# Optimization experiments

Measured on AMD Instinct MI355X. Metric: run time of the kernel, lower is better.

Reference implementation:

```python
import jax, jax.numpy as jnp
import numpy as np

B, S, D, N = 8, 2048, 1024, 1024
RMIN, RMAX = 0.9, 0.999
MAX_PHASE = 6.2831853
EPS = 1e-5


def _ln(v):
    # LayerNorm without affine params (elementwise_affine=False)
    mu = jnp.mean(v, axis=-1, keepdims=True)
    var = jnp.var(v, axis=-1, keepdims=True)
    return (v - mu) * jax.lax.rsqrt(var + EPS)


def setup_inputs() -> dict:
    key = jax.random.key(0)
    ks = jax.random.split(key, 12)
    x = jax.random.normal(ks[0], (B, S, D), dtype=jnp.float32)
    hidden_re = jnp.zeros((B, N), dtype=jnp.float32)
    hidden_im = jnp.zeros((B, N), dtype=jnp.float32)
    # LRU ring initialization (Orvieto et al. 2023)
    u1 = jax.random.uniform(ks[1], (N,), dtype=jnp.float32)
    u2 = jax.random.uniform(ks[2], (N,), dtype=jnp.float32)
    nu_log = jnp.log(-0.5 * jnp.log(u1 * (RMAX**2 - RMIN**2) + RMIN**2))
    theta_log = jnp.log(MAX_PHASE * u2)
    B_re = jax.random.normal(ks[3], (N, D), dtype=jnp.float32) / np.sqrt(2 * D)
    B_im = jax.random.normal(ks[4], (N, D), dtype=jnp.float32) / np.sqrt(2 * D)
    C_re = jax.random.normal(ks[5], (N, N), dtype=jnp.float32) / np.sqrt(N)
    C_im = jax.random.normal(ks[6], (N, N), dtype=jnp.float32) / np.sqrt(N)
    D_skip = jax.random.normal(ks[7], (N, D), dtype=jnp.float32) / np.sqrt(D)
    W_gate = jax.random.normal(ks[8], (N, D), dtype=jnp.float32) / np.sqrt(D)  # gating_proj
    W_con = jax.random.normal(ks[9], (D, N), dtype=jnp.float32) / np.sqrt(N)   # contract
    return {"x": x, "hidden_re": hidden_re, "hidden_im": hidden_im,
            "nu_log": nu_log, "theta_log": theta_log,
            "B_re": B_re, "B_im": B_im, "C_re": C_re, "C_im": C_im,
            "D_skip": D_skip, "W_gate": W_gate, "W_con": W_con}


def reference(x, hidden_re, hidden_im, nu_log, theta_log,
              B_re, B_im, C_re, C_im, D_skip, W_gate, W_con):
    residual = x
    # diagonal complex transition lambda and input normalizer gamma
    mag = jnp.exp(-jnp.exp(nu_log))                 # |lambda|, [N]
    phase = jnp.exp(theta_log)
    lam_re = mag * jnp.cos(phase)
    lam_im = mag * jnp.sin(phase)
    gamma = jnp.sqrt(1.0 - mag * mag)               # sqrt(1-|lambda|^2)
    # input projection (complex), pre-scaled by gamma: [B,S,N]
    u_re = jnp.einsum("bsd,nd->bsn", x, B_re) * gamma
    u_im = jnp.einsum("bsd,nd->bsn", x, B_im) * gamma
    # sequential linear recurrence h_t = lambda * h_{t-1} + u_t (complex)
    def step(h, u):
        h_re, h_im = h
        ur, ui = u
        nr = lam_re * h_re - lam_im * h_im + ur
        ni = lam_re * h_im + lam_im * h_re + ui
        return (nr, ni), (nr, ni)
    (hf_re, hf_im), (hs_re, hs_im) = jax.lax.scan(
        step, (hidden_re, hidden_im),
        (jnp.swapaxes(u_re, 0, 1), jnp.swapaxes(u_im, 0, 1)))  # time-major [S,B,N]
    hs_re = jnp.swapaxes(hs_re, 0, 1)  # [B,S,N]
    hs_im = jnp.swapaxes(hs_im, 0, 1)
    # y = Re(C h) + D x
    y = (jnp.einsum("bsn,mn->bsm", hs_re, C_re)
         - jnp.einsum("bsn,mn->bsm", hs_im, C_im)
         + jnp.einsum("bsd,md->bsm", x, D_skip))
    # gated norm / MLP fusion
    y = _ln(y)                                              # rnn_post_norm
    gate = jax.nn.gelu(_ln(jnp.einsum("bsd,nd->bsn", residual, W_gate)), approximate=False)
    y = y * gate
    y = jax.nn.gelu(_ln(y), approximate=False)              # contract_norm + activation
    out = jnp.einsum("bsn,dn->bsd", y, W_con)               # contract
    return (out, hf_re, hf_im)
```

## Files before the change

kernel.cpp:

```cpp
#include <hip/hip_runtime.h>
#include <math.h>

#define Bsz 8
#define Ssz 2048
#define Dsz 1024
#define Nsz 1024
#define CHUNKS 64
#define CLEN 32
#define Msz (Bsz * Ssz)

typedef unsigned short u16;
typedef __attribute__((ext_vector_type(8))) short short8;
typedef __attribute__((ext_vector_type(4))) float floatx4;

__device__ __forceinline__ float b2f(u16 u) {
    unsigned v = ((unsigned)u) << 16; float f; __builtin_memcpy(&f, &v, 4); return f;
}
__device__ __forceinline__ u16 f2b(float f) {
    unsigned u; __builtin_memcpy(&u, &f, 4);
    unsigned r = u + 0x7fffu + ((u >> 16) & 1u);
    return (u16)(r >> 16);
}

struct CvtJobs {
    const float* src[8];
    u16* dst[8];
    int n4[8];
    float scale[8];
    int blk_start[9];
};

__global__ __launch_bounds__(256)
void cvt_multi(CvtJobs J) {
    int b = blockIdx.x;
    int j = 0;
    #pragma unroll
    for (int t = 0; t < 7; ++t) if (b >= J.blk_start[t + 1]) j = t + 1;
    int i = (b - J.blk_start[j]) * 256 + threadIdx.x;
    if (i < J.n4[j]) {
        float4 v = ((const float4*)J.src[j])[i];
        float s = J.scale[j];
        ushort4 o;
        o.x = f2b(v.x * s); o.y = f2b(v.y * s);
        o.z = f2b(v.z * s); o.w = f2b(v.w * s);
        ((ushort4*)J.dst[j])[i] = o;
    }
}

__global__ void lam_setup(const float* __restrict__ nu_log, const float* __restrict__ theta_log,
                          float* lam_re, float* lam_im, float* gam,
                          float* lamL_re, float* lamL_im) {
    int n = blockIdx.x * 256 + threadIdx.x;
    if (n >= Nsz) return;
    float mag = expf(-expf(nu_log[n]));
    float ph  = expf(theta_log[n]);
    float lr = mag * cosf(ph), li = mag * sinf(ph);
    lam_re[n] = lr; lam_im[n] = li;
    gam[n] = sqrtf(fmaxf(1.0f - mag * mag, 0.0f));
    float ar = lr, ai = li;
    #pragma unroll
    for (int i = 0; i < 5; ++i) { float nr = ar*ar - ai*ai; float ni = 2.0f*ar*ai; ar = nr; ai = ni; }
    lamL_re[n] = ar; lamL_im[n] = ai;
}

#define BM 128
#define BN 128
#define BK 64

struct GemmJob {
    const u16* A0; const u16* W0;
    const u16* A1; const u16* W1;
    const u16* A2; const u16* W2;
    int P;
    float* outF;
    u16*   outB;
    const float* colscale;
};
struct GemmBatch { GemmJob j[3]; };

__global__ __launch_bounds__(256, 2)
void gemm_bt(GemmBatch batch, int M, int N, int K) {
    const GemmJob job = batch.j[blockIdx.z];
    __shared__ u16 As[BM * BK];
    __shared__ u16 Ws[BN * BK];
    const int tid  = threadIdx.x;
    const int wave = tid >> 6, lane = tid & 63;
    const int bm = blockIdx.x, bn = blockIdx.y;
    const int wm = (wave >> 1) * 64, wn = (wave & 1) * 64;

    floatx4 acc[4][4];
    #pragma unroll
    for (int i = 0; i < 4; ++i)
        #pragma unroll
        for (int j = 0; j < 4; ++j) acc[i][j] = (floatx4){0.f, 0.f, 0.f, 0.f};

    const u16* Aps[3] = { job.A0, job.A1, job.A2 };
    const u16* Wps[3] = { job.W0, job.W1, job.W2 };

    const int srow8 = lane >> 3;
    const int scol  = ((lane & 7) ^ srow8) * 8;
    const int frow = lane & 15;
    const int fq   = lane >> 4;
    const int fsw  = frow & 7;

    for (int p = 0; p < job.P; ++p) {
        const u16* A = Aps[p];
        const u16* W = Wps[p];
        const u16* gAb = A + (size_t)(bm * BM + srow8) * K + scol;
        const u16* gWb = W + (size_t)(bn * BN + srow8) * K + scol;
        for (int kk = 0; kk < K; kk += BK) {
            __syncthreads();
            #pragma unroll
            for (int jj = 0; jj < 4; ++jj) {
                const int row0 = wave * 32 + jj * 8;
                const u16* gA = gAb + (size_t)row0 * K + kk;
                const u16* gW = gWb + (size_t)row0 * K + kk;
                u16* lA = As + row0 * BK;
                u16* lW = Ws + row0 * BK;
                __builtin_amdgcn_global_load_lds((const __attribute__((address_space(1))) void*)gA,
                                                 (__attribute__((address_space(3))) void*)lA, 16, 0, 0);
                __builtin_amdgcn_global_load_lds((const __attribute__((address_space(1))) void*)gW,
                                                 (__attribute__((address_space(3))) void*)lW, 16, 0, 0);
            }
            __syncthreads();
            #pragma unroll
            for (int h = 0; h < 2; ++h) {
                const int ca = ((h << 2) | fq) ^ fsw;
                short8 af[4], wf[4];
                #pragma unroll
                for (int i = 0; i < 4; ++i)
                    af[i] = *(const short8*)(As + (wm + i * 16 + frow) * BK + ca * 8);
                #pragma unroll
                for (int i = 0; i < 4; ++i)
                    wf[i] = *(const short8*)(Ws + (wn + i * 16 + frow) * BK + ca * 8);
                #pragma unroll
                for (int mi = 0; mi < 4; ++mi)
                    #pragma unroll
                    for (int ni = 0; ni < 4; ++ni)
                        acc[mi][ni] = __builtin_amdgcn_mfma_f32_16x16x32_bf16(af[mi], wf[ni], acc[mi][ni], 0, 0, 0);
            }
        }
    }

    const int rgrp = lane >> 4;
    const int ccol = lane & 15;
    #pragma unroll
    for (int mi = 0; mi < 4; ++mi) {
        #pragma unroll
        for (int r = 0; r < 4; ++r) {
            int row = bm * BM + wm + mi * 16 + rgrp * 4 + r;
            #pragma unroll
            for (int ni = 0; ni < 4; ++ni) {
                int col = bn * BN + wn + ni * 16 + ccol;
                float v = acc[mi][ni][r];
                if (job.colscale) v *= job.colscale[col];
                size_t idx = (size_t)row * N + col;
                if (job.outF) job.outF[idx] = v;
                else          job.outB[idx] = f2b(v);
            }
        }
    }
}

__global__ void scan_phase1(const u16* __restrict__ u_re, const u16* __restrict__ u_im,
                            const float* __restrict__ lam_re, const float* __restrict__ lam_im,
                            float* __restrict__ carry_re, float* __restrict__ carry_im) {
    int n = blockIdx.x * 256 + threadIdx.x;
    int c = blockIdx.y, b = blockIdx.z;
    float lr = lam_re[n], li = lam_im[n];
    size_t base = ((size_t)b * Ssz + (size_t)c * CLEN) * Nsz + n;
    float hr = 0.f, hi = 0.f;
    #pragma unroll
    for (int t = 0; t < CLEN; ++t) {
        float ur = b2f(u_re[base + (size_t)t * Nsz]);
        float ui = b2f(u_im[base + (size_t)t * Nsz]);
        float nr = fmaf(lr, hr, fmaf(-li, hi, ur));
        float ni = fmaf(lr, hi, fmaf( li, hr, ui));
        hr = nr; hi = ni;
    }
    size_t ci = ((size_t)b * CHUNKS + c) * Nsz + n;
    carry_re[ci] = hr; carry_im[ci] = hi;
}

__global__ void scan_phase2(const float* __restrict__ carry_re, const float* __restrict__ carry_im,
                            const float* __restrict__ lamL_re, const float* __restrict__ lamL_im,
                            const float* __restrict__ hid_re, const float* __restrict__ hid_im,
                            float* __restrict__ entry_re, float* __restrict__ entry_im,
                            float* __restrict__ out_base) {
    int n = blockIdx.x * 256 + threadIdx.x;
    int b = blockIdx.y;
    float Lr = lamL_re[n], Li = lamL_im[n];
    float Hr = hid_re[b * Nsz + n], Hi = hid_im[b * Nsz + n];
    for (int c = 0; c < CHUNKS; ++c) {
        size_t ci = ((size_t)b * CHUNKS + c) * Nsz + n;
        entry_re[ci] = Hr; entry_im[ci] = Hi;
        float cr = carry_re[ci], cim = carry_im[ci];
        float nr = fmaf(Lr, Hr, fmaf(-Li, Hi, cr));
        float ni = fmaf(Lr, Hi, fmaf( Li, Hr, cim));
        Hr = nr; Hi = ni;
    }
    out_base[(size_t)16777216 + (size_t)b * Nsz + n] = Hr;
    out_base[(size_t)16777216 + 8192 + (size_t)b * Nsz + n] = Hi;
}

__global__ void scan_phase3(const u16* __restrict__ u_re, const u16* __restrict__ u_im,
                            const float* __restrict__ lam_re, const float* __restrict__ lam_im,
                            const float* __restrict__ entry_re, const float* __restrict__ entry_im,
                            u16* __restrict__ hs_re, u16* __restrict__ hs_im) {
    int n = blockIdx.x * 256 + threadIdx.x;
    int c = blockIdx.y, b = blockIdx.z;
    float lr = lam_re[n], li = lam_im[n];
    size_t ci = ((size_t)b * CHUNKS + c) * Nsz + n;
    float hr = entry_re[ci], hi = entry_im[ci];
    size_t base = ((size_t)b * Ssz + (size_t)c * CLEN) * Nsz + n;
    #pragma unroll
    for (int t = 0; t < CLEN; ++t) {
        float ur = b2f(u_re[base + (size_t)t * Nsz]);
        float ui = b2f(u_im[base + (size_t)t * Nsz]);
        float nr = fmaf(lr, hr, fmaf(-li, hi, ur));
        float ni = fmaf(lr, hi, fmaf( li, hr, ui));
        hr = nr; hi = ni;
        hs_re[base + (size_t)t * Nsz] = f2b(hr);
        hs_im[base + (size_t)t * Nsz] = f2b(hi);
    }
}

__device__ __forceinline__ float waveReduce(float v) {
    #pragma unroll
    for (int off = 32; off > 0; off >>= 1) v += __shfl_down(v, off, 64);
    return v;
}
__device__ __forceinline__ float gelu_exact(float x) {
    return 0.5f * x * (1.0f + erff(x * 0.70710678118654752f));
}

__global__ __launch_bounds__(256)
void fuse_ln(const u16* __restrict__ y_raw, const u16* __restrict__ gate_pre, u16* __restrict__ y3) {
    int row = blockIdx.x;
    int tid = threadIdx.x;
    int wave = tid >> 6, lane = tid & 63;
    size_t base = (size_t)row * Nsz + tid * 4;
    ushort4 yv = *(const ushort4*)(y_raw + base);
    ushort4 gv = *(const ushort4*)(gate_pre + base);
    float y[4] = { b2f(yv.x), b2f(yv.y), b2f(yv.z), b2f(yv.w) };
    float g[4] = { b2f(gv.x), b2f(gv.y), b2f(gv.z), b2f(gv.w) };

    float sy = 0.f, sy2 = 0.f, sg = 0.f, sg2 = 0.f;
    #pragma unroll
    for (int i = 0; i < 4; ++i) {
        sy += y[i]; sy2 += y[i] * y[i];
        sg += g[i]; sg2 += g[i] * g[i];
    }
    __shared__ float sh[16];
    sy = waveReduce(sy); sy2 = waveReduce(sy2);
    sg = waveReduce(sg); sg2 = waveReduce(sg2);
    if (lane == 0) { sh[wave] = sy; sh[wave + 4] = sy2; sh[wave + 8] = sg; sh[wave + 12] = sg2; }
    __syncthreads();
    sy  = sh[0] + sh[1] + sh[2] + sh[3];
    sy2 = sh[4] + sh[5] + sh[6] + sh[7];
    sg  = sh[8] + sh[9] + sh[10] + sh[11];
    sg2 = sh[12] + sh[13] + sh[14] + sh[15];
    const float inv = 1.0f / (float)Nsz;
    float muy = sy * inv, vary = sy2 * inv - muy * muy, ry = rsqrtf(vary + 1e-5f);
    float mug = sg * inv, varg = sg2 * inv - mug * mug, rg = rsqrtf(varg + 1e-5f);

    float y2[4]; float s2 = 0.f, s22 = 0.f;
    #pragma unroll
    for (int i = 0; i < 4; ++i) {
        float ly = (y[i] - muy) * ry;
        float lg = (g[i] - mug) * rg;
        float t = ly * gelu_exact(lg);
        y2[i] = t; s2 += t; s22 += t * t;
    }
    s2 = waveReduce(s2); s22 = waveReduce(s22);
    __syncthreads();
    if (lane == 0) { sh[wave] = s2; sh[wave + 4] = s22; }
    __syncthreads();
    s2  = sh[0] + sh[1] + sh[2] + sh[3];
    s22 = sh[4] + sh[5] + sh[6] + sh[7];
    float mu2 = s2 * inv, var2 = s22 * inv - mu2 * mu2, r2 = rsqrtf(var2 + 1e-5f);
    ushort4 ov;
    ov.x = f2b(gelu_exact((y2[0] - mu2) * r2));
    ov.y = f2b(gelu_exact((y2[1] - mu2) * r2));
    ov.z = f2b(gelu_exact((y2[2] - mu2) * r2));
    ov.w = f2b(gelu_exact((y2[3] - mu2) * r2));
    *(ushort4*)(y3 + base) = ov;
}

extern "C" void kernel_launch(void* const* d_in, const int* in_sizes, int n_in,
                              void* d_out, int out_size, void* d_ws, size_t ws_size,
                              hipStream_t stream) {
    const float* x         = (const float*)d_in[0];
    const float* hid_re    = (const float*)d_in[1];
    const float* hid_im    = (const float*)d_in[2];
    const float* nu_log    = (const float*)d_in[3];
    const float* theta_log = (const float*)d_in[4];
    const float* B_re      = (const float*)d_in[5];
    const float* B_im      = (const float*)d_in[6];
    const float* C_re      = (const float*)d_in[7];
    const float* C_im      = (const float*)d_in[8];
    const float* D_skip    = (const float*)d_in[9];
    const float* W_gate    = (const float*)d_in[10];
    const float* W_con     = (const float*)d_in[11];
    float* out = (float*)d_out;

    char* ws = (char*)d_ws;
    const size_t MB = 1ull << 20;
    u16* wBre  = (u16*)(ws + 0 * MB);
    u16* wBim  = (u16*)(ws + 2 * MB);
    u16* wCre  = (u16*)(ws + 4 * MB);
    u16* wCimN = (u16*)(ws + 6 * MB);
    u16* wDsk  = (u16*)(ws + 8 * MB);
    u16* wWg   = (u16*)(ws + 10 * MB);
    u16* wWc   = (u16*)(ws + 12 * MB);
    float* lam_re = (float*)(ws + 14 * MB);
    float* lam_im = lam_re + 1024;
    float* gam    = lam_re + 2048;
    float* lamLre = lam_re + 3072;
    float* lamLim = lam_re + 4096;
    u16* xb    = (u16*)(ws + 16 * MB);
    u16* u_re  = (u16*)(ws + 48 * MB);
    u16* u_im  = (u16*)(ws + 80 * MB);
    u16* gate  = (u16*)(ws + 112 * MB);
    u16* hs_re = (u16*)(ws + 144 * MB);
    u16* hs_im = (u16*)(ws + 176 * MB);
    float* carry_re = (float*)(ws + 208 * MB);
    float* carry_im = (float*)(ws + 210 * MB);
    float* entry_re = (float*)(ws + 212 * MB);
    float* entry_im = (float*)(ws + 214 * MB);
    u16* y_raw = u_re;
    u16* y3    = u_im;

    CvtJobs J = {};
    const int WQ = (Nsz * Dsz) / 4;
    const int WB = WQ / 256;
    J.src[0] = x;      J.dst[0] = xb;    J.n4[0] = (Msz * Dsz) / 4; J.scale[0] = 1.0f;
    J.src[1] = B_re;   J.dst[1] = wBre;  J.n4[1] = WQ; J.scale[1] = 1.0f;
    J.src[2] = B_im;   J.dst[2] = wBim;  J.n4[2] = WQ; J.scale[2] = 1.0f;
    J.src[3] = C_re;   J.dst[3] = wCre;  J.n4[3] = WQ; J.scale[3] = 1.0f;
    J.src[4] = C_im;   J.dst[4] = wCimN; J.n4[4] = WQ; J.scale[4] = -1.0f;
    J.src[5] = D_skip; J.dst[5] = wDsk;  J.n4[5] = WQ; J.scale[5] = 1.0f;
    J.src[6] = W_gate; J.dst[6] = wWg;   J.n4[6] = WQ; J.scale[6] = 1.0f;
    J.src[7] = W_con;  J.dst[7] = wWc;   J.n4[7] = WQ; J.scale[7] = 1.0f;
    J.blk_start[0] = 0;
    J.blk_start[1] = 16384;
    for (int t = 2; t <= 8; ++t) J.blk_start[t] = J.blk_start[t - 1] + WB;
    cvt_multi<<<J.blk_start[8], 256, 0, stream>>>(J);
    lam_setup<<<4, 256, 0, stream>>>(nu_log, theta_log, lam_re, lam_im, gam, lamLre, lamLim);

    GemmBatch b1 = {};
    b1.j[0] = { xb, wBre, nullptr, nullptr, nullptr, nullptr, 1, nullptr, u_re, gam };
    b1.j[1] = { xb, wBim, nullptr, nullptr, nullptr, nullptr, 1, nullptr, u_im, gam };
    b1.j[2] = { xb, wWg,  nullptr, nullptr, nullptr, nullptr, 1, nullptr, gate, nullptr };
    gemm_bt<<<dim3(Msz / BM, Nsz / BN, 3), 256, 0, stream>>>(b1, Msz, Nsz, Dsz);

    scan_phase1<<<dim3(Nsz / 256, CHUNKS, Bsz), 256, 0, stream>>>(u_re, u_im, lam_re, lam_im, carry_re, carry_im);
    scan_phase2<<<dim3(Nsz / 256, Bsz), 256, 0, stream>>>(carry_re, carry_im, lamLre, lamLim,
                                                          hid_re, hid_im, entry_re, entry_im, out);
    scan_phase3<<<dim3(Nsz / 256, CHUNKS, Bsz), 256, 0, stream>>>(u_re, u_im, lam_re, lam_im,
                                                                  entry_re, entry_im, hs_re, hs_im);

    GemmBatch b2 = {};
    b2.j[0] = { hs_re, wCre, hs_im, wCimN, xb, wDsk, 3, nullptr, y_raw, nullptr };
    gemm_bt<<<dim3(Msz / BM, Nsz / BN, 1), 256, 0, stream>>>(b2, Msz, Nsz, Nsz);

    fuse_ln<<<Msz, 256, 0, stream>>>(y_raw, gate, y3);

    GemmBatch b3 = {};
    b3.j[0] = { y3, wWc, nullptr, nullptr, nullptr, nullptr, 1, out, nullptr, nullptr };
    gemm_bt<<<dim3(Msz / BM, Dsz / BN, 1), 256, 0, stream>>>(b3, Msz, Dsz, Nsz);

    (void)in_sizes; (void)n_in; (void)out_size; (void)ws_size;
}
```

Measured before the change: 505.0 us.

## Double-buffer GEMM LDS tiles with BK=32 and vectorize scan kernels

```diff
diff --git a/kernel.cpp b/kernel.cpp
--- a/kernel.cpp
+++ b/kernel.cpp
@@ -8,6 +8,7 @@
 #define CHUNKS 64
 #define CLEN 32
 #define Msz (Bsz * Ssz)
+#define Ksz 1024
 
 typedef unsigned short u16;
 typedef __attribute__((ext_vector_type(8))) short short8;
@@ -65,7 +66,8 @@
 
 #define BM 128
 #define BN 128
-#define BK 64
+#define BK 32
+#define KITER 32
 
 struct GemmJob {
     const u16* A0; const u16* W0;
@@ -78,11 +80,11 @@
 };
 struct GemmBatch { GemmJob j[3]; };
 
-__global__ __launch_bounds__(256, 2)
-void gemm_bt(GemmBatch batch, int M, int N, int K) {
+__global__ __launch_bounds__(256, 3)
+void gemm_bt(GemmBatch batch) {
     const GemmJob job = batch.j[blockIdx.z];
-    __shared__ u16 As[BM * BK];
-    __shared__ u16 Ws[BN * BK];
+    __shared__ u16 As[2][BM * BK];
+    __shared__ u16 Ws[2][BN * BK];
     const int tid  = threadIdx.x;
     const int wave = tid >> 6, lane = tid & 63;
     const int bm = blockIdx.x, bn = blockIdx.y;
@@ -96,50 +98,61 @@
 
     const u16* Aps[3] = { job.A0, job.A1, job.A2 };
     const u16* Wps[3] = { job.W0, job.W1, job.W2 };
-
-    const int srow8 = lane >> 3;
-    const int scol  = ((lane & 7) ^ srow8) * 8;
+    const int TOT = job.P * KITER;
+
+    const int srow = wave * 32 + (lane >> 2);
+    const int scol = ((lane & 3) ^ ((lane >> 3) & 3)) * 8;
+    const size_t sAoff = (size_t)(bm * BM + srow) * Ksz + scol;
+    const size_t sWoff = (size_t)(bn * BN + srow) * Ksz + scol;
     const int frow = lane & 15;
-    const int fq   = lane >> 4;
-    const int fsw  = frow & 7;
-
-    for (int p = 0; p < job.P; ++p) {
-        const u16* A = Aps[p];
-        const u16* W = Wps[p];
-        const u16* gAb = A + (size_t)(bm * BM + srow8) * K + scol;
-        const u16* gWb = W + (size_t)(bn * BN + srow8) * K + scol;
-        for (int kk = 0; kk < K; kk += BK) {
-            __syncthreads();
+    const int fk   = (((lane >> 4) ^ ((frow >> 1) & 3))) * 8;
+
+    {
+        const u16* gA = Aps[0] + sAoff;
+        const u16* gW = Wps[0] + sWoff;
+        #pragma unroll
+        for (int jj = 0; jj < 2; ++jj) {
+            u16* lA = &As[0][(wave * 32 + jj * 16) * BK];
+            u16* lW = &Ws[0][(wave * 32 + jj * 16) * BK];
+            __builtin_amdgcn_global_load_lds((const __attribute__((address_space(1))) void*)(gA + (size_t)(jj * 16) * Ksz),
+                                             (__attribute__((address_space(3))) void*)lA, 16, 0, 0);
+            __builtin_amdgcn_global_load_lds((const __attribute__((address_space(1))) void*)(gW + (size_t)(jj * 16) * Ksz),
+                                             (__attribute__((address_space(3))) void*)lW, 16, 0, 0);
+        }
+    }
+
+    for (int i = 0; i < TOT; ++i) {
+        const int cur = i & 1;
+        __syncthreads();
+        if (i + 1 < TOT) {
+            const int ni = i + 1;
+            const int p = ni >> 5;
+            const int koff = (ni & 31) * BK;
+            const u16* gA = Aps[p] + sAoff + koff;
+            const u16* gW = Wps[p] + sWoff + koff;
+            const int nb = cur ^ 1;
             #pragma unroll
-            for (int jj = 0; jj < 4; ++jj) {
-                const int row0 = wave * 32 + jj * 8;
-                const u16* gA = gAb + (size_t)row0 * K + kk;
-                const u16* gW = gWb + (size_t)row0 * K + kk;
-                u16* lA = As + row0 * BK;
-                u16* lW = Ws + row0 * BK;
-                __builtin_amdgcn_global_load_lds((const __attribute__((address_space(1))) void*)gA,
+            for (int jj = 0; jj < 2; ++jj) {
+                u16* lA = &As[nb][(wave * 32 + jj * 16) * BK];
+                u16* lW = &Ws[nb][(wave * 32 + jj * 16) * BK];
+                __builtin_amdgcn_global_load_lds((const __attribute__((address_space(1))) void*)(gA + (size_t)(jj * 16) * Ksz),
                                                  (__attribute__((address_space(3))) void*)lA, 16, 0, 0);
-                __builtin_amdgcn_global_load_lds((const __attribute__((address_space(1))) void*)gW,
+                __builtin_amdgcn_global_load_lds((const __attribute__((address_space(1))) void*)(gW + (size_t)(jj * 16) * Ksz),
                                                  (__attribute__((address_space(3))) void*)lW, 16, 0, 0);
             }
-            __syncthreads();
+        }
+        short8 af[4], wf[4];
+        #pragma unroll
+        for (int t = 0; t < 4; ++t)
+            af[t] = *(const short8*)(&As[cur][(wm + t * 16 + frow) * BK + fk]);
+        #pragma unroll
+        for (int t = 0; t < 4; ++t)
+            wf[t] = *(const short8*)(&Ws[cur][(wn + t * 16 + frow) * BK + fk]);
+        #pragma unroll
+        for (int mi = 0; mi < 4; ++mi)
             #pragma unroll
-            for (int h = 0; h < 2; ++h) {
-                const int ca = ((h << 2) | fq) ^ fsw;
-                short8 af[4], wf[4];
-                #pragma unroll
-                for (int i = 0; i < 4; ++i)
-                    af[i] = *(const short8*)(As + (wm + i * 16 + frow) * BK + ca * 8);
-                #pragma unroll
-                for (int i = 0; i < 4; ++i)
-                    wf[i] = *(const short8*)(Ws + (wn + i * 16 + frow) * BK + ca * 8);
-                #pragma unroll
-                for (int mi = 0; mi < 4; ++mi)
-                    #pragma unroll
-                    for (int ni = 0; ni < 4; ++ni)
-                        acc[mi][ni] = __builtin_amdgcn_mfma_f32_16x16x32_bf16(af[mi], wf[ni], acc[mi][ni], 0, 0, 0);
-            }
-        }
+            for (int ni2 = 0; ni2 < 4; ++ni2)
+                acc[mi][ni2] = __builtin_amdgcn_mfma_f32_16x16x32_bf16(af[mi], wf[ni2], acc[mi][ni2], 0, 0, 0);
     }
 
     const int rgrp = lane >> 4;
@@ -154,7 +167,7 @@
                 int col = bn * BN + wn + ni * 16 + ccol;
                 float v = acc[mi][ni][r];
                 if (job.colscale) v *= job.colscale[col];
-                size_t idx = (size_t)row * N + col;
+                size_t idx = (size_t)row * Nsz + col;
                 if (job.outF) job.outF[idx] = v;
                 else          job.outB[idx] = f2b(v);
             }
@@ -165,21 +178,29 @@
 __global__ void scan_phase1(const u16* __restrict__ u_re, const u16* __restrict__ u_im,
                             const float* __restrict__ lam_re, const float* __restrict__ lam_im,
                             float* __restrict__ carry_re, float* __restrict__ carry_im) {
-    int n = blockIdx.x * 256 + threadIdx.x;
-    int c = blockIdx.y, b = blockIdx.z;
-    float lr = lam_re[n], li = lam_im[n];
+    int n = threadIdx.x * 4;
+    int c = blockIdx.x, b = blockIdx.y;
+    float4 lr = *(const float4*)(lam_re + n);
+    float4 li = *(const float4*)(lam_im + n);
     size_t base = ((size_t)b * Ssz + (size_t)c * CLEN) * Nsz + n;
-    float hr = 0.f, hi = 0.f;
+    float hr[4] = {0.f, 0.f, 0.f, 0.f}, hi[4] = {0.f, 0.f, 0.f, 0.f};
+    const float* lrp = (const float*)&lr; const float* lip = (const float*)&li;
     #pragma unroll
     for (int t = 0; t < CLEN; ++t) {
-        float ur = b2f(u_re[base + (size_t)t * Nsz]);
-        float ui = b2f(u_im[base + (size_t)t * Nsz]);
-        float nr = fmaf(lr, hr, fmaf(-li, hi, ur));
-        float ni = fmaf(lr, hi, fmaf( li, hr, ui));
-        hr = nr; hi = ni;
+        ushort4 urv = *(const ushort4*)(u_re + base + (size_t)t * Nsz);
+        ushort4 uiv = *(const ushort4*)(u_im + base + (size_t)t * Nsz);
+        float ur[4] = { b2f(urv.x), b2f(urv.y), b2f(urv.z), b2f(urv.w) };
+        float ui[4] = { b2f(uiv.x), b2f(uiv.y), b2f(uiv.z), b2f(uiv.w) };
+        #pragma unroll
+        for (int q = 0; q < 4; ++q) {
+            float nr = fmaf(lrp[q], hr[q], fmaf(-lip[q], hi[q], ur[q]));
+            float ni = fmaf(lrp[q], hi[q], fmaf( lip[q], hr[q], ui[q]));
+            hr[q] = nr; hi[q] = ni;
+        }
     }
     size_t ci = ((size_t)b * CHUNKS + c) * Nsz + n;
-    carry_re[ci] = hr; carry_im[ci] = hi;
+    *(float4*)(carry_re + ci) = (float4){hr[0], hr[1], hr[2], hr[3]};
+    *(float4*)(carry_im + ci) = (float4){hi[0], hi[1], hi[2], hi[3]};
 }
 
 __global__ void scan_phase2(const float* __restrict__ carry_re, const float* __restrict__ carry_im,
@@ -207,21 +228,33 @@
                             const float* __restrict__ lam_re, const float* __restrict__ lam_im,
                             const float* __restrict__ entry_re, const float* __restrict__ entry_im,
                             u16* __restrict__ hs_re, u16* __restrict__ hs_im) {
-    int n = blockIdx.x * 256 + threadIdx.x;
-    int c = blockIdx.y, b = blockIdx.z;
-    float lr = lam_re[n], li = lam_im[n];
+    int n = threadIdx.x * 4;
+    int c = blockIdx.x, b = blockIdx.y;
+    float4 lr = *(const float4*)(lam_re + n);
+    float4 li = *(const float4*)(lam_im + n);
+    const float* lrp = (const float*)&lr; const float* lip = (const float*)&li;
     size_t ci = ((size_t)b * CHUNKS + c) * Nsz + n;
-    float hr = entry_re[ci], hi = entry_im[ci];
+    float4 er = *(const float4*)(entry_re + ci);
+    float4 ei = *(const float4*)(entry_im + ci);
+    float hr[4] = {er.x, er.y, er.z, er.w}, hi[4] = {ei.x, ei.y, ei.z, ei.w};
     size_t base = ((size_t)b * Ssz + (size_t)c * CLEN) * Nsz + n;
     #pragma unroll
     for (int t = 0; t < CLEN; ++t) {
-        float ur = b2f(u_re[base + (size_t)t * Nsz]);
-        float ui = b2f(u_im[base + (size_t)t * Nsz]);
-        float nr = fmaf(lr, hr, fmaf(-li, hi, ur));
-        float ni = fmaf(lr, hi, fmaf( li, hr, ui));
-        hr = nr; hi = ni;
-        hs_re[base + (size_t)t * Nsz] = f2b(hr);
-        hs_im[base + (size_t)t * Nsz] = f2b(hi);
+        ushort4 urv = *(const ushort4*)(u_re + base + (size_t)t * Nsz);
+        ushort4 uiv = *(const ushort4*)(u_im + base + (size_t)t * Nsz);
+        float ur[4] = { b2f(urv.x), b2f(urv.y), b2f(urv.z), b2f(urv.w) };
+        float ui[4] = { b2f(uiv.x), b2f(uiv.y), b2f(uiv.z), b2f(uiv.w) };
+        ushort4 orv, oiv;
+        u16* orp = (u16*)&orv; u16* oip = (u16*)&oiv;
+        #pragma unroll
+        for (int q = 0; q < 4; ++q) {
+            float nr = fmaf(lrp[q], hr[q], fmaf(-lip[q], hi[q], ur[q]));
+            float ni = fmaf(lrp[q], hi[q], fmaf( lip[q], hr[q], ui[q]));
+            hr[q] = nr; hi[q] = ni;
+            orp[q] = f2b(nr); oip[q] = f2b(ni);
+        }
+        *(ushort4*)(hs_re + base + (size_t)t * Nsz) = orv;
+        *(ushort4*)(hs_im + base + (size_t)t * Nsz) = oiv;
     }
 }
 
@@ -352,23 +385,23 @@
     b1.j[0] = { xb, wBre, nullptr, nullptr, nullptr, nullptr, 1, nullptr, u_re, gam };
     b1.j[1] = { xb, wBim, nullptr, nullptr, nullptr, nullptr, 1, nullptr, u_im, gam };
     b1.j[2] = { xb, wWg,  nullptr, nullptr, nullptr, nullptr, 1, nullptr, gate, nullptr };
-    gemm_bt<<<dim3(Msz / BM, Nsz / BN, 3), 256, 0, stream>>>(b1, Msz, Nsz, Dsz);
-
-    scan_phase1<<<dim3(Nsz / 256, CHUNKS, Bsz), 256, 0, stream>>>(u_re, u_im, lam_re, lam_im, carry_re, carry_im);
+    gemm_bt<<<dim3(Msz / BM, Nsz / BN, 3), 256, 0, stream>>>(b1);
+
+    scan_phase1<<<dim3(CHUNKS, Bsz), 256, 0, stream>>>(u_re, u_im, lam_re, lam_im, carry_re, carry_im);
     scan_phase2<<<dim3(Nsz / 256, Bsz), 256, 0, stream>>>(carry_re, carry_im, lamLre, lamLim,
                                                           hid_re, hid_im, entry_re, entry_im, out);
-    scan_phase3<<<dim3(Nsz / 256, CHUNKS, Bsz), 256, 0, stream>>>(u_re, u_im, lam_re, lam_im,
-                                                                  entry_re, entry_im, hs_re, hs_im);
+    scan_phase3<<<dim3(CHUNKS, Bsz), 256, 0, stream>>>(u_re, u_im, lam_re, lam_im,
+                                                       entry_re, entry_im, hs_re, hs_im);
 
     GemmBatch b2 = {};
     b2.j[0] = { hs_re, wCre, hs_im, wCimN, xb, wDsk, 3, nullptr, y_raw, nullptr };
-    gemm_bt<<<dim3(Msz / BM, Nsz / BN, 1), 256, 0, stream>>>(b2, Msz, Nsz, Nsz);
+    gemm_bt<<<dim3(Msz / BM, Nsz / BN, 1), 256, 0, stream>>>(b2);
 
     fuse_ln<<<Msz, 256, 0, stream>>>(y_raw, gate, y3);
 
     GemmBatch b3 = {};
     b3.j[0] = { y3, wWc, nullptr, nullptr, nullptr, nullptr, 1, out, nullptr, nullptr };
-    gemm_bt<<<dim3(Msz / BM, Dsz / BN, 1), 256, 0, stream>>>(b3, Msz, Dsz, Nsz);
+    gemm_bt<<<dim3(Msz / BM, Dsz / BN, 1), 256, 0, stream>>>(b3);
 
     (void)in_sizes; (void)n_in; (void)out_size; (void)ws_size;
 }
```

After: 523.6 us. +3.7%, slower.
